# Kernel optimization log

Measured on AMD Instinct MI355X. Metric: run time of the kernel, lower is better.

Reference implementation:

```python
import jax, jax.numpy as jnp
import numpy as np

N = 50000      # nodes
E = 800000     # edges (avg degree 16)
G = 500        # graphs in batch
D = 128        # emb_dim
ED = 7         # edge_dim
L = 5          # num_layers
C = 10         # num_class
BN_EPS = 1e-5


def _bn(x, g, b, m, v):
    # BatchNorm1d in eval mode: running stats
    return (x - m) * jax.lax.rsqrt(v + BN_EPS) * g + b


def setup_inputs() -> dict:
    key = jax.random.key(0)
    ks = jax.random.split(key, 32)
    f32 = jnp.float32
    edge_attr = jax.random.normal(ks[0], (E, ED), f32)
    edge_index = jax.random.randint(ks[1], (2, E), 0, N)
    batch = jnp.sort(jax.random.randint(ks[2], (N,), 0, G))

    w = lambda k, shp, s: jax.random.normal(k, shp, f32) * s
    s_in = 1.0 / np.sqrt(D)
    node_emb = w(ks[3], (1, D), 1.0)
    edge_W = w(ks[4], (L, ED, D), 1.0 / np.sqrt(ED))
    edge_b = w(ks[5], (L, D), 0.01)
    mlp_W1 = w(ks[6], (L, D, D), s_in)
    mlp_b1 = w(ks[7], (L, D), 0.01)
    mlp_W2 = w(ks[8], (L, D, D), s_in)
    mlp_b2 = w(ks[9], (L, D), 0.01)
    bn1_g = jax.random.uniform(ks[10], (L, D), f32, 0.5, 1.5)
    bn1_b = w(ks[11], (L, D), 0.1)
    bn1_m = w(ks[12], (L, D), 0.1)
    bn1_v = jax.random.uniform(ks[13], (L, D), f32, 0.5, 1.5)
    bn2_g = jax.random.uniform(ks[14], (L, D), f32, 0.5, 1.5)
    bn2_b = w(ks[15], (L, D), 0.1)
    bn2_m = w(ks[16], (L, D), 0.1)
    bn2_v = jax.random.uniform(ks[17], (L, D), f32, 0.5, 1.5)
    head_W1 = w(ks[18], (D, D), s_in)
    head_b1 = w(ks[19], (D,), 0.01)
    head_W2 = w(ks[20], (D, C), s_in)
    head_b2 = w(ks[21], (C,), 0.01)
    return dict(edge_attr=edge_attr, edge_index=edge_index, batch=batch,
                node_emb=node_emb, edge_W=edge_W, edge_b=edge_b,
                mlp_W1=mlp_W1, mlp_b1=mlp_b1, bn1_g=bn1_g, bn1_b=bn1_b,
                bn1_m=bn1_m, bn1_v=bn1_v, mlp_W2=mlp_W2, mlp_b2=mlp_b2,
                bn2_g=bn2_g, bn2_b=bn2_b, bn2_m=bn2_m, bn2_v=bn2_v,
                head_W1=head_W1, head_b1=head_b1, head_W2=head_W2, head_b2=head_b2)


def reference(edge_attr, edge_index, batch, node_emb, edge_W, edge_b,
              mlp_W1, mlp_b1, bn1_g, bn1_b, bn1_m, bn1_v,
              mlp_W2, mlp_b2, bn2_g, bn2_b, bn2_m, bn2_v,
              head_W1, head_b1, head_W2, head_b2):
    src, dst = edge_index[0], edge_index[1]
    # node_emb indexed by zeros -> every node starts with the same row
    x = jnp.broadcast_to(node_emb[0], (N, D))
    for l in range(L):
        # GINEConv: msg_ij = relu(x_j + Lin(edge_attr_ij)); aggr = sum over in-edges
        e = edge_attr @ edge_W[l] + edge_b[l]               # [E, D]
        msg = jax.nn.relu(x[src] + e)                       # gather + add + relu
        agg = jax.ops.segment_sum(msg, dst, num_segments=N) # scatter-add
        h = x + agg                                         # (1 + eps) * x, eps = 0
        # inner MLP: Linear -> BN -> ReLU -> Linear
        h = h @ mlp_W1[l] + mlp_b1[l]
        h = jax.nn.relu(_bn(h, bn1_g[l], bn1_b[l], bn1_m[l], bn1_v[l]))
        h = h @ mlp_W2[l] + mlp_b2[l]
        # outer BN + ReLU (dropout identity in eval)
        x = jax.nn.relu(_bn(h, bn2_g[l], bn2_b[l], bn2_m[l], bn2_v[l]))
    # global mean pool over graphs
    counts = jnp.maximum(jax.ops.segment_sum(jnp.ones((N,), x.dtype), batch, num_segments=G), 1.0)
    g = jax.ops.segment_sum(x, batch, num_segments=G) / counts[:, None]
    # head: Linear -> ReLU -> (Dropout) -> Linear
    h = jax.nn.relu(g @ head_W1 + head_b1)
    return h @ head_W2 + head_b2
```

## Files before the change

kernel.cpp:

```cpp
#include <hip/hip_runtime.h>

#define N_NODES 50000
#define N_PAD   50048
#define N_EDGES 800000
#define N_GRAPHS 500
#define DIM 128
#define EDIM 7
#define LAYERS 5
#define NCLASS 10
#define BN_EPS 1e-5f
#define TM 64
#define AST 264
#define NSB ((N_NODES + 256) / 256)
#define NBA 16

typedef __attribute__((ext_vector_type(8))) short bf16x8;
typedef __attribute__((ext_vector_type(4))) float f32x4;
typedef _Float16 h2 __attribute__((ext_vector_type(2)));

struct __align__(32) ERec { uint4 ea; int src; int pad0, pad1, pad2; };

__device__ __forceinline__ unsigned short f2bf(float f) {
    unsigned u = __float_as_uint(f);
    u = u + 0x7fffu + ((u >> 16) & 1u);
    return (unsigned short)(u >> 16);
}
__device__ __forceinline__ float bf2f(unsigned short h) {
    return __uint_as_float(((unsigned)h) << 16);
}
__device__ __forceinline__ h2 u2h2(unsigned u) {
    union { unsigned u; h2 h; } c; c.u = u; return c.h;
}
__device__ __forceinline__ unsigned h22u(h2 h) {
    union { h2 h; unsigned u; } c; c.h = h; return c.u;
}
__device__ __forceinline__ unsigned packh2(float a, float b) {
    h2 h; h.x = (_Float16)a; h.y = (_Float16)b;
    return h22u(h);
}


__global__ void zero_ints(int* __restrict__ p, int n) {
    int i = blockIdx.x * 256 + threadIdx.x;
    if (i < n) p[i] = 0;
}

__global__ void hist_kernel(const int* __restrict__ dst, int* __restrict__ deg) {
    int e = blockIdx.x * 256 + threadIdx.x;
    if (e < N_EDGES) atomicAdd(&deg[dst[e]], 1);
}

__global__ __launch_bounds__(256)
void scan1(const int* __restrict__ deg, int* __restrict__ ro, int* __restrict__ bsums) {
    __shared__ int ws[4];
    int t = threadIdx.x;
    int i = blockIdx.x * 256 + t;
    int v = (i < N_NODES) ? deg[i] : 0;
    int lane = t & 63, wv = t >> 6;
    int s = v;
    #pragma unroll
    for (int off = 1; off < 64; off <<= 1) {
        int u = __shfl_up(s, off, 64);
        if (lane >= off) s += u;
    }
    if (lane == 63) ws[wv] = s;
    __syncthreads();
    if (t == 0) {
        int a = 0;
        #pragma unroll
        for (int k = 0; k < 4; ++k) { int x = ws[k]; ws[k] = a; a += x; }
        bsums[blockIdx.x] = a;
    }
    __syncthreads();
    int excl = s - v + ws[wv];
    if (i <= N_NODES) ro[i] = excl;
}

__global__ __launch_bounds__(256)
void scan2(int* __restrict__ bsums) {
    __shared__ int ws[4];
    int t = threadIdx.x;
    int v = (t < NSB) ? bsums[t] : 0;
    int lane = t & 63, wv = t >> 6;
    int s = v;
    #pragma unroll
    for (int off = 1; off < 64; off <<= 1) {
        int u = __shfl_up(s, off, 64);
        if (lane >= off) s += u;
    }
    if (lane == 63) ws[wv] = s;
    __syncthreads();
    if (t == 0) {
        int a = 0;
        #pragma unroll
        for (int k = 0; k < 4; ++k) { int x = ws[k]; ws[k] = a; a += x; }
    }
    __syncthreads();
    if (t < NSB) bsums[t] = s - v + ws[wv];
}

__global__ __launch_bounds__(256)
void scan3(int* __restrict__ ro, const int* __restrict__ bsums, int* __restrict__ cursor) {
    int i = blockIdx.x * 256 + threadIdx.x;
    if (i <= N_NODES) {
        int r = ro[i] + bsums[i >> 8];
        ro[i] = r;
        if (i < N_NODES) cursor[i] = r;
    }
}

__global__ void fill_rec(const int* __restrict__ dst, const int* __restrict__ src,
                         const float* __restrict__ edge_attr,
                         int* __restrict__ cursor, ERec* __restrict__ rec) {
    int e = blockIdx.x * 256 + threadIdx.x;
    if (e < N_EDGES) {
        const float* ap = edge_attr + (size_t)e * EDIM;
        uint4 ea;
        ea.x = packh2(ap[0], ap[1]);
        ea.y = packh2(ap[2], ap[3]);
        ea.z = packh2(ap[4], ap[5]);
        ea.w = packh2(ap[6], 0.f);
        int s = src[e];
        int pos = atomicAdd(&cursor[dst[e]], 1);
        rec[pos].ea = ea;
        rec[pos].src = s;
    }
}


__global__ void init_x(float* __restrict__ x, unsigned short* __restrict__ xb,
                       const float* __restrict__ emb) {
    int i = blockIdx.x * 256 + threadIdx.x;
    if (i < N_NODES * DIM) {
        float v = emb[i & (DIM - 1)];
        x[i] = v;
        xb[i] = f2bf(v);
    }
}

__global__ void prep_w(const float* __restrict__ W1, const float* __restrict__ W2,
                       unsigned short* __restrict__ Wthi, unsigned short* __restrict__ Wtlo) {
    int i = blockIdx.x * 256 + threadIdx.x;
    if (i >= 2 * LAYERS * DIM * DIM) return;
    int m = i >> 14;
    int n = i & 127;
    int k = (i >> 7) & 127;
    const float* W = (m < LAYERS) ? (W1 + (size_t)m * DIM * DIM)
                                  : (W2 + (size_t)(m - LAYERS) * DIM * DIM);
    float v = W[k * DIM + n];
    unsigned short hi = f2bf(v);
    float lo = v - bf2f(hi);
    size_t o = ((size_t)m << 14) + (size_t)n * DIM + k;
    Wthi[o] = hi;
    Wtlo[o] = f2bf(lo);
}


#if __has_builtin(__builtin_amdgcn_fdot2)
#define HAVE_FDOT2 1
#else
#define HAVE_FDOT2 0
#endif

__device__ __forceinline__ void edge_accum8(float4& acc0, float4& acc1,
                                            uint4 eav, uint4 xv,
                                            const unsigned* Wp,
                                            const float4& b0, const float4& b1) {
    float el[8] = {b0.x, b0.y, b0.z, b0.w, b1.x, b1.y, b1.z, b1.w};
#if HAVE_FDOT2
    #pragma unroll
    for (int d = 0; d < 8; ++d) {
        float e = el[d];
        e = __builtin_amdgcn_fdot2(u2h2(eav.x), u2h2(Wp[d * 4 + 0]), e, false);
        e = __builtin_amdgcn_fdot2(u2h2(eav.y), u2h2(Wp[d * 4 + 1]), e, false);
        e = __builtin_amdgcn_fdot2(u2h2(eav.z), u2h2(Wp[d * 4 + 2]), e, false);
        e = __builtin_amdgcn_fdot2(u2h2(eav.w), u2h2(Wp[d * 4 + 3]), e, false);
        el[d] = e;
    }
#else
    h2 ea01 = u2h2(eav.x), ea23 = u2h2(eav.y), ea45 = u2h2(eav.z), ea67 = u2h2(eav.w);
    float a[8] = {(float)ea01.x, (float)ea01.y, (float)ea23.x, (float)ea23.y,
                  (float)ea45.x, (float)ea45.y, (float)ea67.x, 0.f};
    #pragma unroll
    for (int d = 0; d < 8; ++d) {
        float e = el[d];
        #pragma unroll
        for (int kp = 0; kp < 4; ++kp) {
            h2 w = u2h2(Wp[d * 4 + kp]);
            e += a[kp * 2] * (float)w.x + a[kp * 2 + 1] * (float)w.y;
        }
        el[d] = e;
    }
#endif
    acc0.x += fmaxf(__uint_as_float(xv.x << 16)         + el[0], 0.f);
    acc0.y += fmaxf(__uint_as_float(xv.x & 0xffff0000u) + el[1], 0.f);
    acc0.z += fmaxf(__uint_as_float(xv.y << 16)         + el[2], 0.f);
    acc0.w += fmaxf(__uint_as_float(xv.y & 0xffff0000u) + el[3], 0.f);
    acc1.x += fmaxf(__uint_as_float(xv.z << 16)         + el[4], 0.f);
    acc1.y += fmaxf(__uint_as_float(xv.z & 0xffff0000u) + el[5], 0.f);
    acc1.z += fmaxf(__uint_as_float(xv.w << 16)         + el[6], 0.f);
    acc1.w += fmaxf(__uint_as_float(xv.w & 0xffff0000u) + el[7], 0.f);
}

__global__ __launch_bounds__(256, 4)
void aggregate(const float* __restrict__ x, const unsigned short* __restrict__ xb,
               float* __restrict__ h,
               const ERec* __restrict__ rec,
               const int* __restrict__ row_off,
               const float* __restrict__ eW, const float* __restrict__ eb) {
    int t = threadIdx.x;
    int nl = t >> 4, lane = t & 15, c0 = lane * 8;
    int n = blockIdx.x * NBA + nl;

    unsigned Wp[32];
    #pragma unroll
    for (int d = 0; d < 8; ++d) {
        #pragma unroll
        for (int kp = 0; kp < 4; ++kp) {
            float w0 = eW[(kp * 2) * DIM + c0 + d];
            float w1 = (kp * 2 + 1 < EDIM) ? eW[(kp * 2 + 1) * DIM + c0 + d] : 0.f;
            Wp[d * 4 + kp] = packh2(w0, w1);
        }
    }
    float4 b0 = *reinterpret_cast<const float4*>(eb + c0);
    float4 b1 = *reinterpret_cast<const float4*>(eb + c0 + 4);
    #pragma unroll
    for (int k = 0; k < 32; ++k) asm volatile("" : "+v"(Wp[k]));
    asm volatile("" : "+v"(b0.x), "+v"(b0.y), "+v"(b0.z), "+v"(b0.w));
    asm volatile("" : "+v"(b1.x), "+v"(b1.y), "+v"(b1.z), "+v"(b1.w));

    float4 acc0 = *reinterpret_cast<const float4*>(x + (size_t)n * DIM + c0);
    float4 acc1 = *reinterpret_cast<const float4*>(x + (size_t)n * DIM + c0 + 4);
    int idx = row_off[n], end = row_off[n + 1];

    int s_c[4];
    bool have = (idx + 4 <= end);
    if (have) {
        #pragma unroll
        for (int j = 0; j < 4; ++j) s_c[j] = rec[idx + j].src;
    }
    while (have) {
        uint4 ea[4], xv[4];
        #pragma unroll
        for (int j = 0; j < 4; ++j) ea[j] = rec[idx + j].ea;
        #pragma unroll
        for (int j = 0; j < 4; ++j) xv[j] = *reinterpret_cast<const uint4*>(xb + (size_t)s_c[j] * DIM + c0);
        idx += 4;
        bool nxt = (idx + 4 <= end);
        int s_n[4];
        if (nxt) {
            #pragma unroll
            for (int j = 0; j < 4; ++j) s_n[j] = rec[idx + j].src;
        }
        #pragma unroll
        for (int j = 0; j < 4; ++j) edge_accum8(acc0, acc1, ea[j], xv[j], Wp, b0, b1);
        if (nxt) {
            #pragma unroll
            for (int j = 0; j < 4; ++j) s_c[j] = s_n[j];
        }
        have = nxt;
    }
    for (; idx < end; ++idx) {
        int s = rec[idx].src;
        uint4 ea = rec[idx].ea;
        uint4 xv = *reinterpret_cast<const uint4*>(xb + (size_t)s * DIM + c0);
        edge_accum8(acc0, acc1, ea, xv, Wp, b0, b1);
    }
    *reinterpret_cast<float4*>(h + (size_t)n * DIM + c0) = acc0;
    *reinterpret_cast<float4*>(h + (size_t)n * DIM + c0 + 4) = acc1;
}


__global__ __launch_bounds__(256)
void gemm2x(const float* __restrict__ in, float* __restrict__ outx,
            unsigned short* __restrict__ xb_out,
            const unsigned short* __restrict__ W1hi, const unsigned short* __restrict__ W1lo,
            const unsigned short* __restrict__ W2hi, const unsigned short* __restrict__ W2lo,
            const float* __restrict__ b1,
            const float* __restrict__ bn1g, const float* __restrict__ bn1b,
            const float* __restrict__ bn1m, const float* __restrict__ bn1v,
            const float* __restrict__ b2,
            const float* __restrict__ bn2g, const float* __restrict__ bn2b,
            const float* __restrict__ bn2m, const float* __restrict__ bn2v) {
    __shared__ __align__(16) unsigned short A2[TM * AST];
    int t = threadIdx.x;
    int r0 = blockIdx.x * TM;
    int w = t >> 6;
    int lane = t & 63;
    int q = lane >> 4;
    int l16 = lane & 15;

    bf16x8 bh[2][4], bl[2][4];
    #pragma unroll
    for (int nt = 0; nt < 2; ++nt) {
        int n = w * 32 + nt * 16 + l16;
        const bf16x8* gh = reinterpret_cast<const bf16x8*>(W1hi + (size_t)n * DIM);
        const bf16x8* gl = reinterpret_cast<const bf16x8*>(W1lo + (size_t)n * DIM);
        #pragma unroll
        for (int kc = 0; kc < 4; ++kc) {
            bh[nt][kc] = gh[kc * 4 + q];
            bl[nt][kc] = gl[kc * 4 + q];
        }
    }

    #pragma unroll
    for (int i = 0; i < 8; ++i) {
        int idx = t + i * 256;
        int row = idx >> 5;
        int kp = (idx & 31) * 4;
        float4 v = reinterpret_cast<const float4*>(in + (size_t)r0 * DIM)[idx];
        unsigned short h0 = f2bf(v.x), h1 = f2bf(v.y), h2_ = f2bf(v.z), h3 = f2bf(v.w);
        ushort4 hv; hv.x = h0; hv.y = h1; hv.z = h2_; hv.w = h3;
        ushort4 lv;
        lv.x = f2bf(v.x - bf2f(h0)); lv.y = f2bf(v.y - bf2f(h1));
        lv.z = f2bf(v.z - bf2f(h2_)); lv.w = f2bf(v.w - bf2f(h3));
        *reinterpret_cast<ushort4*>(&A2[row * AST + kp]) = hv;
        *reinterpret_cast<ushort4*>(&A2[row * AST + 128 + kp]) = lv;
    }
    __syncthreads();

    f32x4 acc[4][2];
    #pragma unroll
    for (int mt = 0; mt < 4; ++mt)
        #pragma unroll
        for (int nt = 0; nt < 2; ++nt)
            acc[mt][nt] = (f32x4){0.f, 0.f, 0.f, 0.f};

    #pragma unroll
    for (int kc = 0; kc < 4; ++kc) {
        bf16x8 ahi[4], alo[4];
        #pragma unroll
        for (int mt = 0; mt < 4; ++mt) {
            ahi[mt] = *reinterpret_cast<const bf16x8*>(&A2[(mt * 16 + l16) * AST + kc * 32 + q * 8]);
            alo[mt] = *reinterpret_cast<const bf16x8*>(&A2[(mt * 16 + l16) * AST + 128 + kc * 32 + q * 8]);
        }
        #pragma unroll
        for (int mt = 0; mt < 4; ++mt)
            #pragma unroll
            for (int nt = 0; nt < 2; ++nt) {
                acc[mt][nt] = __builtin_amdgcn_mfma_f32_16x16x32_bf16(ahi[mt], bh[nt][kc], acc[mt][nt], 0, 0, 0);
                acc[mt][nt] = __builtin_amdgcn_mfma_f32_16x16x32_bf16(ahi[mt], bl[nt][kc], acc[mt][nt], 0, 0, 0);
                acc[mt][nt] = __builtin_amdgcn_mfma_f32_16x16x32_bf16(alo[mt], bh[nt][kc], acc[mt][nt], 0, 0, 0);
            }
    }
    __syncthreads();

    #pragma unroll
    for (int nt = 0; nt < 2; ++nt) {
        int n = w * 32 + nt * 16 + l16;
        const bf16x8* gh = reinterpret_cast<const bf16x8*>(W2hi + (size_t)n * DIM);
        const bf16x8* gl = reinterpret_cast<const bf16x8*>(W2lo + (size_t)n * DIM);
        #pragma unroll
        for (int kc = 0; kc < 4; ++kc) {
            bh[nt][kc] = gh[kc * 4 + q];
            bl[nt][kc] = gl[kc * 4 + q];
        }
    }

    #pragma unroll
    for (int nt = 0; nt < 2; ++nt) {
        int col = w * 32 + nt * 16 + l16;
        float bias = b1[col];
        float sc = bn1g[col] * rsqrtf(bn1v[col] + BN_EPS);
        float sh = bn1b[col] - bn1m[col] * sc;
        #pragma unroll
        for (int mt = 0; mt < 4; ++mt) {
            #pragma unroll
            for (int r = 0; r < 4; ++r) {
                int rowl = mt * 16 + q * 4 + r;
                float o = fmaxf((acc[mt][nt][r] + bias) * sc + sh, 0.f);
                unsigned short hi = f2bf(o);
                A2[rowl * AST + col] = hi;
                A2[rowl * AST + 128 + col] = f2bf(o - bf2f(hi));
            }
        }
    }
    __syncthreads();

    #pragma unroll
    for (int mt = 0; mt < 4; ++mt)
        #pragma unroll
        for (int nt = 0; nt < 2; ++nt)
            acc[mt][nt] = (f32x4){0.f, 0.f, 0.f, 0.f};

    #pragma unroll
    for (int kc = 0; kc < 4; ++kc) {
        bf16x8 ahi[4], alo[4];
        #pragma unroll
        for (int mt = 0; mt < 4; ++mt) {
            ahi[mt] = *reinterpret_cast<const bf16x8*>(&A2[(mt * 16 + l16) * AST + kc * 32 + q * 8]);
            alo[mt] = *reinterpret_cast<const bf16x8*>(&A2[(mt * 16 + l16) * AST + 128 + kc * 32 + q * 8]);
        }
        #pragma unroll
        for (int mt = 0; mt < 4; ++mt)
            #pragma unroll
            for (int nt = 0; nt < 2; ++nt) {
                acc[mt][nt] = __builtin_amdgcn_mfma_f32_16x16x32_bf16(ahi[mt], bh[nt][kc], acc[mt][nt], 0, 0, 0);
                acc[mt][nt] = __builtin_amdgcn_mfma_f32_16x16x32_bf16(ahi[mt], bl[nt][kc], acc[mt][nt], 0, 0, 0);
                acc[mt][nt] = __builtin_amdgcn_mfma_f32_16x16x32_bf16(alo[mt], bh[nt][kc], acc[mt][nt], 0, 0, 0);
            }
    }

    #pragma unroll
    for (int nt = 0; nt < 2; ++nt) {
        int col = w * 32 + nt * 16 + l16;
        float bias = b2[col];
        float sc = bn2g[col] * rsqrtf(bn2v[col] + BN_EPS);
        float sh = bn2b[col] - bn2m[col] * sc;
        #pragma unroll
        for (int mt = 0; mt < 4; ++mt) {
            #pragma unroll
            for (int r = 0; r < 4; ++r) {
                int row = r0 + mt * 16 + q * 4 + r;
                float o = fmaxf((acc[mt][nt][r] + bias) * sc + sh, 0.f);
                outx[(size_t)row * DIM + col] = o;
                xb_out[(size_t)row * DIM + col] = f2bf(o);
            }
        }
    }
}


__global__ __launch_bounds__(256)
void pool_kernel(const float* __restrict__ x, const int* __restrict__ batch,
                 float* __restrict__ g) {
    __shared__ float sh[256];
    __shared__ int sb[2];
    int gid = blockIdx.x;
    int t = threadIdx.x;
    if (t < 2) {
        int tgt = gid + t;
        int lo = 0, hi = N_NODES;
        while (lo < hi) { int mid = (lo + hi) >> 1; if (batch[mid] < tgt) lo = mid + 1; else hi = mid; }
        sb[t] = lo;
    }
    __syncthreads();
    int lo = sb[0], hi = sb[1];
    int d = t & 127, half = t >> 7;
    float a = 0.f;
    for (int n = lo + half; n < hi; n += 2) a += x[(size_t)n * DIM + d];
    sh[t] = a;
    __syncthreads();
    if (t < DIM) {
        float cnt = fmaxf((float)(hi - lo), 1.f);
        g[gid * DIM + t] = (sh[t] + sh[t + 128]) / cnt;
    }
}


__global__ __launch_bounds__(128)
void head1_kernel(const float* __restrict__ g, const float* __restrict__ W1,
                  const float* __restrict__ b1, float* __restrict__ h1) {
    __shared__ float gs[DIM];
    int gid = blockIdx.x, c = threadIdx.x;
    gs[c] = g[gid * DIM + c];
    __syncthreads();
    float acc = b1[c];
    for (int k = 0; k < DIM; ++k) acc += gs[k] * W1[k * DIM + c];
    h1[gid * DIM + c] = fmaxf(acc, 0.f);
}

__global__ __launch_bounds__(64)
void head2_kernel(const float* __restrict__ h1, const float* __restrict__ W2,
                  const float* __restrict__ b2, float* __restrict__ out) {
    __shared__ float hs[DIM];
    int gid = blockIdx.x;
    int t = threadIdx.x;
    hs[t] = h1[gid * DIM + t];
    hs[t + 64] = h1[gid * DIM + t + 64];
    __syncthreads();
    if (t < NCLASS) {
        float acc = b2[t];
        for (int k = 0; k < DIM; ++k) acc += hs[k] * W2[k * NCLASS + t];
        out[gid * NCLASS + t] = acc;
    }
}


extern "C" void kernel_launch(void* const* d_in, const int* in_sizes, int n_in,
                              void* d_out, int out_size, void* d_ws, size_t ws_size,
                              hipStream_t stream) {
    const float* edge_attr = (const float*)d_in[0];
    const int*   edge_index = (const int*)d_in[1];
    const int*   batch = (const int*)d_in[2];
    const float* node_emb = (const float*)d_in[3];
    const float* edge_W = (const float*)d_in[4];
    const float* edge_b = (const float*)d_in[5];
    const float* mlp_W1 = (const float*)d_in[6];
    const float* mlp_b1 = (const float*)d_in[7];
    const float* bn1_g = (const float*)d_in[8];
    const float* bn1_b = (const float*)d_in[9];
    const float* bn1_m = (const float*)d_in[10];
    const float* bn1_v = (const float*)d_in[11];
    const float* mlp_W2 = (const float*)d_in[12];
    const float* mlp_b2 = (const float*)d_in[13];
    const float* bn2_g = (const float*)d_in[14];
    const float* bn2_b = (const float*)d_in[15];
    const float* bn2_m = (const float*)d_in[16];
    const float* bn2_v = (const float*)d_in[17];
    const float* head_W1 = (const float*)d_in[18];
    const float* head_b1 = (const float*)d_in[19];
    const float* head_W2 = (const float*)d_in[20];
    const float* head_b2 = (const float*)d_in[21];
    float* out = (float*)d_out;

    const int* src = edge_index;
    const int* dst = edge_index + N_EDGES;

    size_t off = 0;
    auto carve = [&](size_t bytes) {
        void* p = (char*)d_ws + off;
        off += (bytes + 255) & ~(size_t)255;
        return p;
    };
    float* x            = (float*)carve((size_t)N_PAD * DIM * 4);
    unsigned short* xb  = (unsigned short*)carve((size_t)N_PAD * DIM * 2);
    float* h            = (float*)carve((size_t)N_PAD * DIM * 4);
    ERec* rec           = (ERec*)carve((size_t)N_EDGES * sizeof(ERec));
    unsigned short* Wthi = (unsigned short*)carve((size_t)2 * LAYERS * DIM * DIM * 2);
    unsigned short* Wtlo = (unsigned short*)carve((size_t)2 * LAYERS * DIM * DIM * 2);
    int* deg      = (int*)carve((size_t)N_NODES * 4);
    int* row_off  = (int*)carve((size_t)(N_NODES + 1) * 4);
    int* cursor   = (int*)carve((size_t)N_NODES * 4);
    int* bsums    = (int*)carve((size_t)NSB * 4);
    float* gbuf   = (float*)carve((size_t)N_GRAPHS * DIM * 4);
    float* h1buf  = (float*)carve((size_t)N_GRAPHS * DIM * 4);
    (void)ws_size;

    zero_ints<<<(N_NODES + 255) / 256, 256, 0, stream>>>(deg, N_NODES);
    hist_kernel<<<(N_EDGES + 255) / 256, 256, 0, stream>>>(dst, deg);
    scan1<<<NSB, 256, 0, stream>>>(deg, row_off, bsums);
    scan2<<<1, 256, 0, stream>>>(bsums);
    scan3<<<NSB, 256, 0, stream>>>(row_off, bsums, cursor);
    fill_rec<<<(N_EDGES + 255) / 256, 256, 0, stream>>>(dst, src, edge_attr, cursor, rec);

    init_x<<<(N_NODES * DIM + 255) / 256, 256, 0, stream>>>(x, xb, node_emb);
    prep_w<<<(2 * LAYERS * DIM * DIM + 255) / 256, 256, 0, stream>>>(mlp_W1, mlp_W2, Wthi, Wtlo);

    const int gemm_blocks = N_PAD / TM;
    for (int l = 0; l < LAYERS; ++l) {
        aggregate<<<N_NODES / NBA, 256, 0, stream>>>(
            x, xb, h, rec, row_off,
            edge_W + (size_t)l * EDIM * DIM, edge_b + (size_t)l * DIM);
        gemm2x<<<gemm_blocks, 256, 0, stream>>>(
            h, x, xb,
            Wthi + ((size_t)l << 14), Wtlo + ((size_t)l << 14),
            Wthi + ((size_t)(LAYERS + l) << 14), Wtlo + ((size_t)(LAYERS + l) << 14),
            mlp_b1 + (size_t)l * DIM,
            bn1_g + (size_t)l * DIM, bn1_b + (size_t)l * DIM,
            bn1_m + (size_t)l * DIM, bn1_v + (size_t)l * DIM,
            mlp_b2 + (size_t)l * DIM,
            bn2_g + (size_t)l * DIM, bn2_b + (size_t)l * DIM,
            bn2_m + (size_t)l * DIM, bn2_v + (size_t)l * DIM);
    }

    pool_kernel<<<N_GRAPHS, 256, 0, stream>>>(x, batch, gbuf);
    head1_kernel<<<N_GRAPHS, 128, 0, stream>>>(gbuf, head_W1, head_b1, h1buf);
    head2_kernel<<<N_GRAPHS, 64, 0, stream>>>(h1buf, head_W2, head_b2, out);
}
```

Baseline: 606.6 us.

## Split node edge lists across two half-groups, SoA edge records, stream GEMM weights

The edge record struct is split into a packed 16-byte attribute array and a separate source-index array, removing the 32-byte padded records. The aggregate kernel now assigns 32 threads per node, each half handling half of the in-edges, and combines the two halves with a shuffle reduction. This doubles parallelism per node at the cost of a simpler two-way unrolled loop in place of the previous four-deep software-pipelined one. The GEMM kernel also loads weight fragments per k-chunk with one-ahead prefetch rather than holding all of them in registers, and sets launch bounds to 3 waves to raise occupancy.

```diff
diff --git a/kernel.cpp b/kernel.cpp
--- a/kernel.cpp
+++ b/kernel.cpp
@@ -12,13 +12,10 @@
 #define TM 64
 #define AST 264
 #define NSB ((N_NODES + 256) / 256)
-#define NBA 16
 
 typedef __attribute__((ext_vector_type(8))) short bf16x8;
 typedef __attribute__((ext_vector_type(4))) float f32x4;
 typedef _Float16 h2 __attribute__((ext_vector_type(2)));
-
-struct __align__(32) ERec { uint4 ea; int src; int pad0, pad1, pad2; };
 
 __device__ __forceinline__ unsigned short f2bf(float f) {
     unsigned u = __float_as_uint(f);
@@ -111,7 +108,8 @@
 
 __global__ void fill_rec(const int* __restrict__ dst, const int* __restrict__ src,
                          const float* __restrict__ edge_attr,
-                         int* __restrict__ cursor, ERec* __restrict__ rec) {
+                         int* __restrict__ cursor,
+                         uint4* __restrict__ ea16, int* __restrict__ srcc) {
     int e = blockIdx.x * 256 + threadIdx.x;
     if (e < N_EDGES) {
         const float* ap = edge_attr + (size_t)e * EDIM;
@@ -122,8 +120,8 @@
         ea.w = packh2(ap[6], 0.f);
         int s = src[e];
         int pos = atomicAdd(&cursor[dst[e]], 1);
-        rec[pos].ea = ea;
-        rec[pos].src = s;
+        ea16[pos] = ea;
+        srcc[pos] = s;
     }
 }
 
@@ -205,12 +203,17 @@
 __global__ __launch_bounds__(256, 4)
 void aggregate(const float* __restrict__ x, const unsigned short* __restrict__ xb,
                float* __restrict__ h,
-               const ERec* __restrict__ rec,
+               const uint4* __restrict__ ea16,
+               const int* __restrict__ srcc,
                const int* __restrict__ row_off,
                const float* __restrict__ eW, const float* __restrict__ eb) {
     int t = threadIdx.x;
-    int nl = t >> 4, lane = t & 15, c0 = lane * 8;
-    int n = blockIdx.x * NBA + nl;
+    int g = t >> 5;
+    int lane32 = t & 31;
+    int half = lane32 >> 4;
+    int l16 = lane32 & 15;
+    int c0 = l16 * 8;
+    int n = blockIdx.x * 8 + g;
 
     unsigned Wp[32];
     #pragma unroll
@@ -229,49 +232,51 @@
     asm volatile("" : "+v"(b0.x), "+v"(b0.y), "+v"(b0.z), "+v"(b0.w));
     asm volatile("" : "+v"(b1.x), "+v"(b1.y), "+v"(b1.z), "+v"(b1.w));
 
-    float4 acc0 = *reinterpret_cast<const float4*>(x + (size_t)n * DIM + c0);
-    float4 acc1 = *reinterpret_cast<const float4*>(x + (size_t)n * DIM + c0 + 4);
-    int idx = row_off[n], end = row_off[n + 1];
-
-    int s_c[4];
-    bool have = (idx + 4 <= end);
-    if (have) {
-        #pragma unroll
-        for (int j = 0; j < 4; ++j) s_c[j] = rec[idx + j].src;
-    }
-    while (have) {
-        uint4 ea[4], xv[4];
-        #pragma unroll
-        for (int j = 0; j < 4; ++j) ea[j] = rec[idx + j].ea;
-        #pragma unroll
-        for (int j = 0; j < 4; ++j) xv[j] = *reinterpret_cast<const uint4*>(xb + (size_t)s_c[j] * DIM + c0);
-        idx += 4;
-        bool nxt = (idx + 4 <= end);
-        int s_n[4];
-        if (nxt) {
-            #pragma unroll
-            for (int j = 0; j < 4; ++j) s_n[j] = rec[idx + j].src;
-        }
-        #pragma unroll
-        for (int j = 0; j < 4; ++j) edge_accum8(acc0, acc1, ea[j], xv[j], Wp, b0, b1);
-        if (nxt) {
-            #pragma unroll
-            for (int j = 0; j < 4; ++j) s_c[j] = s_n[j];
-        }
-        have = nxt;
-    }
-    for (; idx < end; ++idx) {
-        int s = rec[idx].src;
-        uint4 ea = rec[idx].ea;
-        uint4 xv = *reinterpret_cast<const uint4*>(xb + (size_t)s * DIM + c0);
-        edge_accum8(acc0, acc1, ea, xv, Wp, b0, b1);
-    }
-    *reinterpret_cast<float4*>(h + (size_t)n * DIM + c0) = acc0;
-    *reinterpret_cast<float4*>(h + (size_t)n * DIM + c0 + 4) = acc1;
-}
-
-
-__global__ __launch_bounds__(256)
+    float4 acc0, acc1;
+    if (half == 0) {
+        acc0 = *reinterpret_cast<const float4*>(x + (size_t)n * DIM + c0);
+        acc1 = *reinterpret_cast<const float4*>(x + (size_t)n * DIM + c0 + 4);
+    } else {
+        acc0 = make_float4(0.f, 0.f, 0.f, 0.f);
+        acc1 = make_float4(0.f, 0.f, 0.f, 0.f);
+    }
+
+    int beg = row_off[n], end = row_off[n + 1];
+    int mid = beg + ((end - beg + 1) >> 1);
+    int idx  = half ? mid : beg;
+    int stop = half ? end : mid;
+
+    for (; idx + 2 <= stop; idx += 2) {
+        int s0 = srcc[idx], s1 = srcc[idx + 1];
+        uint4 ea0 = ea16[idx], ea1 = ea16[idx + 1];
+        uint4 xv0 = *reinterpret_cast<const uint4*>(xb + (size_t)s0 * DIM + c0);
+        uint4 xv1 = *reinterpret_cast<const uint4*>(xb + (size_t)s1 * DIM + c0);
+        edge_accum8(acc0, acc1, ea0, xv0, Wp, b0, b1);
+        edge_accum8(acc0, acc1, ea1, xv1, Wp, b0, b1);
+    }
+    if (idx < stop) {
+        int s0 = srcc[idx];
+        uint4 ea0 = ea16[idx];
+        uint4 xv0 = *reinterpret_cast<const uint4*>(xb + (size_t)s0 * DIM + c0);
+        edge_accum8(acc0, acc1, ea0, xv0, Wp, b0, b1);
+    }
+
+    acc0.x += __shfl_xor(acc0.x, 16, 32);
+    acc0.y += __shfl_xor(acc0.y, 16, 32);
+    acc0.z += __shfl_xor(acc0.z, 16, 32);
+    acc0.w += __shfl_xor(acc0.w, 16, 32);
+    acc1.x += __shfl_xor(acc1.x, 16, 32);
+    acc1.y += __shfl_xor(acc1.y, 16, 32);
+    acc1.z += __shfl_xor(acc1.z, 16, 32);
+    acc1.w += __shfl_xor(acc1.w, 16, 32);
+    if (half == 0) {
+        *reinterpret_cast<float4*>(h + (size_t)n * DIM + c0) = acc0;
+        *reinterpret_cast<float4*>(h + (size_t)n * DIM + c0 + 4) = acc1;
+    }
+}
+
+
+__global__ __launch_bounds__(256, 3)
 void gemm2x(const float* __restrict__ in, float* __restrict__ outx,
             unsigned short* __restrict__ xb_out,
             const unsigned short* __restrict__ W1hi, const unsigned short* __restrict__ W1lo,
@@ -289,18 +294,14 @@
     int lane = t & 63;
     int q = lane >> 4;
     int l16 = lane & 15;
-
-    bf16x8 bh[2][4], bl[2][4];
+    int nfr0 = w * 32 + l16;
+
+    bf16x8 cbh[2], cbl[2];
     #pragma unroll
     for (int nt = 0; nt < 2; ++nt) {
-        int n = w * 32 + nt * 16 + l16;
-        const bf16x8* gh = reinterpret_cast<const bf16x8*>(W1hi + (size_t)n * DIM);
-        const bf16x8* gl = reinterpret_cast<const bf16x8*>(W1lo + (size_t)n * DIM);
-        #pragma unroll
-        for (int kc = 0; kc < 4; ++kc) {
-            bh[nt][kc] = gh[kc * 4 + q];
-            bl[nt][kc] = gl[kc * 4 + q];
-        }
+        size_t o = (size_t)(nfr0 + nt * 16) * DIM + q * 8;
+        cbh[nt] = *reinterpret_cast<const bf16x8*>(W1hi + o);
+        cbl[nt] = *reinterpret_cast<const bf16x8*>(W1lo + o);
     }
 
     #pragma unroll
@@ -328,6 +329,15 @@
 
     #pragma unroll
     for (int kc = 0; kc < 4; ++kc) {
+        bf16x8 nbh[2], nbl[2];
+        if (kc < 3) {
+            #pragma unroll
+            for (int nt = 0; nt < 2; ++nt) {
+                size_t o = (size_t)(nfr0 + nt * 16) * DIM + (kc + 1) * 32 + q * 8;
+                nbh[nt] = *reinterpret_cast<const bf16x8*>(W1hi + o);
+                nbl[nt] = *reinterpret_cast<const bf16x8*>(W1lo + o);
+            }
+        }
         bf16x8 ahi[4], alo[4];
         #pragma unroll
         for (int mt = 0; mt < 4; ++mt) {
@@ -338,23 +348,22 @@
         for (int mt = 0; mt < 4; ++mt)
             #pragma unroll
             for (int nt = 0; nt < 2; ++nt) {
-                acc[mt][nt] = __builtin_amdgcn_mfma_f32_16x16x32_bf16(ahi[mt], bh[nt][kc], acc[mt][nt], 0, 0, 0);
-                acc[mt][nt] = __builtin_amdgcn_mfma_f32_16x16x32_bf16(ahi[mt], bl[nt][kc], acc[mt][nt], 0, 0, 0);
-                acc[mt][nt] = __builtin_amdgcn_mfma_f32_16x16x32_bf16(alo[mt], bh[nt][kc], acc[mt][nt], 0, 0, 0);
+                acc[mt][nt] = __builtin_amdgcn_mfma_f32_16x16x32_bf16(ahi[mt], cbh[nt], acc[mt][nt], 0, 0, 0);
+                acc[mt][nt] = __builtin_amdgcn_mfma_f32_16x16x32_bf16(ahi[mt], cbl[nt], acc[mt][nt], 0, 0, 0);
+                acc[mt][nt] = __builtin_amdgcn_mfma_f32_16x16x32_bf16(alo[mt], cbh[nt], acc[mt][nt], 0, 0, 0);
             }
+        if (kc < 3) {
+            #pragma unroll
+            for (int nt = 0; nt < 2; ++nt) { cbh[nt] = nbh[nt]; cbl[nt] = nbl[nt]; }
+        }
     }
     __syncthreads();
 
     #pragma unroll
     for (int nt = 0; nt < 2; ++nt) {
-        int n = w * 32 + nt * 16 + l16;
-        const bf16x8* gh = reinterpret_cast<const bf16x8*>(W2hi + (size_t)n * DIM);
-        const bf16x8* gl = reinterpret_cast<const bf16x8*>(W2lo + (size_t)n * DIM);
-        #pragma unroll
-        for (int kc = 0; kc < 4; ++kc) {
-            bh[nt][kc] = gh[kc * 4 + q];
-            bl[nt][kc] = gl[kc * 4 + q];
-        }
+        size_t o = (size_t)(nfr0 + nt * 16) * DIM + q * 8;
+        cbh[nt] = *reinterpret_cast<const bf16x8*>(W2hi + o);
+        cbl[nt] = *reinterpret_cast<const bf16x8*>(W2lo + o);
     }
 
     #pragma unroll
@@ -385,6 +394,15 @@
 
     #pragma unroll
     for (int kc = 0; kc < 4; ++kc) {
+        bf16x8 nbh[2], nbl[2];
+        if (kc < 3) {
+            #pragma unroll
+            for (int nt = 0; nt < 2; ++nt) {
+                size_t o = (size_t)(nfr0 + nt * 16) * DIM + (kc + 1) * 32 + q * 8;
+                nbh[nt] = *reinterpret_cast<const bf16x8*>(W2hi + o);
+                nbl[nt] = *reinterpret_cast<const bf16x8*>(W2lo + o);
+            }
+        }
         bf16x8 ahi[4], alo[4];
         #pragma unroll
         for (int mt = 0; mt < 4; ++mt) {
@@ -395,10 +413,14 @@
         for (int mt = 0; mt < 4; ++mt)
             #pragma unroll
             for (int nt = 0; nt < 2; ++nt) {
-                acc[mt][nt] = __builtin_amdgcn_mfma_f32_16x16x32_bf16(ahi[mt], bh[nt][kc], acc[mt][nt], 0, 0, 0);
-                acc[mt][nt] = __builtin_amdgcn_mfma_f32_16x16x32_bf16(ahi[mt], bl[nt][kc], acc[mt][nt], 0, 0, 0);
-                acc[mt][nt] = __builtin_amdgcn_mfma_f32_16x16x32_bf16(alo[mt], bh[nt][kc], acc[mt][nt], 0, 0, 0);
+                acc[mt][nt] = __builtin_amdgcn_mfma_f32_16x16x32_bf16(ahi[mt], cbh[nt], acc[mt][nt], 0, 0, 0);
+                acc[mt][nt] = __builtin_amdgcn_mfma_f32_16x16x32_bf16(ahi[mt], cbl[nt], acc[mt][nt], 0, 0, 0);
+                acc[mt][nt] = __builtin_amdgcn_mfma_f32_16x16x32_bf16(alo[mt], cbh[nt], acc[mt][nt], 0, 0, 0);
             }
+        if (kc < 3) {
+            #pragma unroll
+            for (int nt = 0; nt < 2; ++nt) { cbh[nt] = nbh[nt]; cbl[nt] = nbl[nt]; }
+        }
     }
 
     #pragma unroll
@@ -516,7 +538,8 @@
     float* x            = (float*)carve((size_t)N_PAD * DIM * 4);
     unsigned short* xb  = (unsigned short*)carve((size_t)N_PAD * DIM * 2);
     float* h            = (float*)carve((size_t)N_PAD * DIM * 4);
-    ERec* rec           = (ERec*)carve((size_t)N_EDGES * sizeof(ERec));
+    uint4* ea16         = (uint4*)carve((size_t)N_EDGES * 16);
+    int* srcc           = (int*)carve((size_t)N_EDGES * 4);
     unsigned short* Wthi = (unsigned short*)carve((size_t)2 * LAYERS * DIM * DIM * 2);
     unsigned short* Wtlo = (unsigned short*)carve((size_t)2 * LAYERS * DIM * DIM * 2);
     int* deg      = (int*)carve((size_t)N_NODES * 4);
@@ -532,15 +555,15 @@
     scan1<<<NSB, 256, 0, stream>>>(deg, row_off, bsums);
     scan2<<<1, 256, 0, stream>>>(bsums);
     scan3<<<NSB, 256, 0, stream>>>(row_off, bsums, cursor);
-    fill_rec<<<(N_EDGES + 255) / 256, 256, 0, stream>>>(dst, src, edge_attr, cursor, rec);
+    fill_rec<<<(N_EDGES + 255) / 256, 256, 0, stream>>>(dst, src, edge_attr, cursor, ea16, srcc);
 
     init_x<<<(N_NODES * DIM + 255) / 256, 256, 0, stream>>>(x, xb, node_emb);
     prep_w<<<(2 * LAYERS * DIM * DIM + 255) / 256, 256, 0, stream>>>(mlp_W1, mlp_W2, Wthi, Wtlo);
 
     const int gemm_blocks = N_PAD / TM;
     for (int l = 0; l < LAYERS; ++l) {
-        aggregate<<<N_NODES / NBA, 256, 0, stream>>>(
-            x, xb, h, rec, row_off,
+        aggregate<<<N_NODES / 8, 256, 0, stream>>>(
+            x, xb, h, ea16, srcc, row_off,
             edge_W + (size_t)l * EDIM * DIM, edge_b + (size_t)l * DIM);
         gemm2x<<<gemm_blocks, 256, 0, stream>>>(
             h, x, xb,
```

Result: slower. 643.1 us (+6.0%).

## Remap aggregate to one wavefront per node with two channels per lane

Applied to the files above, without the earlier changes.

Restructures the edge aggregation kernel so that each 64-lane wavefront handles one destination node, with each lane owning two feature channels, instead of sixteen lanes per node each owning eight channels. Per-lane register use drops from 32 packed edge weights to 8, and launch bounds rise to 8 waves per SIMD to raise occupancy for the latency-bound gather. In exchange, every lane now loads the full edge record and runs its own fdot2 edge projection, so edge-record traffic and redundant edge-linear work per node grow. The explicit four-edge software prefetch of source indices is replaced by a simpler two-edge unroll.

```diff
diff --git a/kernel.cpp b/kernel.cpp
--- a/kernel.cpp
+++ b/kernel.cpp
@@ -12,7 +12,6 @@
 #define TM 64
 #define AST 264
 #define NSB ((N_NODES + 256) / 256)
-#define NBA 16
 
 typedef __attribute__((ext_vector_type(8))) short bf16x8;
 typedef __attribute__((ext_vector_type(4))) float f32x4;
@@ -162,112 +161,82 @@
 #define HAVE_FDOT2 0
 #endif
 
-__device__ __forceinline__ void edge_accum8(float4& acc0, float4& acc1,
-                                            uint4 eav, uint4 xv,
-                                            const unsigned* Wp,
-                                            const float4& b0, const float4& b1) {
-    float el[8] = {b0.x, b0.y, b0.z, b0.w, b1.x, b1.y, b1.z, b1.w};
+__device__ __forceinline__ void edge_accum2(float& acc0, float& acc1,
+                                            uint4 eav, unsigned xv,
+                                            const unsigned* Wp0, const unsigned* Wp1,
+                                            float b0, float b1) {
+    float e0 = b0, e1 = b1;
 #if HAVE_FDOT2
-    #pragma unroll
-    for (int d = 0; d < 8; ++d) {
-        float e = el[d];
-        e = __builtin_amdgcn_fdot2(u2h2(eav.x), u2h2(Wp[d * 4 + 0]), e, false);
-        e = __builtin_amdgcn_fdot2(u2h2(eav.y), u2h2(Wp[d * 4 + 1]), e, false);
-        e = __builtin_amdgcn_fdot2(u2h2(eav.z), u2h2(Wp[d * 4 + 2]), e, false);
-        e = __builtin_amdgcn_fdot2(u2h2(eav.w), u2h2(Wp[d * 4 + 3]), e, false);
-        el[d] = e;
-    }
+    e0 = __builtin_amdgcn_fdot2(u2h2(eav.x), u2h2(Wp0[0]), e0, false);
+    e0 = __builtin_amdgcn_fdot2(u2h2(eav.y), u2h2(Wp0[1]), e0, false);
+    e0 = __builtin_amdgcn_fdot2(u2h2(eav.z), u2h2(Wp0[2]), e0, false);
+    e0 = __builtin_amdgcn_fdot2(u2h2(eav.w), u2h2(Wp0[3]), e0, false);
+    e1 = __builtin_amdgcn_fdot2(u2h2(eav.x), u2h2(Wp1[0]), e1, false);
+    e1 = __builtin_amdgcn_fdot2(u2h2(eav.y), u2h2(Wp1[1]), e1, false);
+    e1 = __builtin_amdgcn_fdot2(u2h2(eav.z), u2h2(Wp1[2]), e1, false);
+    e1 = __builtin_amdgcn_fdot2(u2h2(eav.w), u2h2(Wp1[3]), e1, false);
 #else
     h2 ea01 = u2h2(eav.x), ea23 = u2h2(eav.y), ea45 = u2h2(eav.z), ea67 = u2h2(eav.w);
     float a[8] = {(float)ea01.x, (float)ea01.y, (float)ea23.x, (float)ea23.y,
                   (float)ea45.x, (float)ea45.y, (float)ea67.x, 0.f};
     #pragma unroll
-    for (int d = 0; d < 8; ++d) {
-        float e = el[d];
-        #pragma unroll
-        for (int kp = 0; kp < 4; ++kp) {
-            h2 w = u2h2(Wp[d * 4 + kp]);
-            e += a[kp * 2] * (float)w.x + a[kp * 2 + 1] * (float)w.y;
-        }
-        el[d] = e;
+    for (int kp = 0; kp < 4; ++kp) {
+        h2 w0 = u2h2(Wp0[kp]), w1 = u2h2(Wp1[kp]);
+        e0 += a[kp * 2] * (float)w0.x + a[kp * 2 + 1] * (float)w0.y;
+        e1 += a[kp * 2] * (float)w1.x + a[kp * 2 + 1] * (float)w1.y;
     }
 #endif
-    acc0.x += fmaxf(__uint_as_float(xv.x << 16)         + el[0], 0.f);
-    acc0.y += fmaxf(__uint_as_float(xv.x & 0xffff0000u) + el[1], 0.f);
-    acc0.z += fmaxf(__uint_as_float(xv.y << 16)         + el[2], 0.f);
-    acc0.w += fmaxf(__uint_as_float(xv.y & 0xffff0000u) + el[3], 0.f);
-    acc1.x += fmaxf(__uint_as_float(xv.z << 16)         + el[4], 0.f);
-    acc1.y += fmaxf(__uint_as_float(xv.z & 0xffff0000u) + el[5], 0.f);
-    acc1.z += fmaxf(__uint_as_float(xv.w << 16)         + el[6], 0.f);
-    acc1.w += fmaxf(__uint_as_float(xv.w & 0xffff0000u) + el[7], 0.f);
-}
-
-__global__ __launch_bounds__(256, 4)
+    acc0 += fmaxf(__uint_as_float(xv << 16)         + e0, 0.f);
+    acc1 += fmaxf(__uint_as_float(xv & 0xffff0000u) + e1, 0.f);
+}
+
+__global__ __launch_bounds__(256, 8)
 void aggregate(const float* __restrict__ x, const unsigned short* __restrict__ xb,
                float* __restrict__ h,
                const ERec* __restrict__ rec,
                const int* __restrict__ row_off,
                const float* __restrict__ eW, const float* __restrict__ eb) {
     int t = threadIdx.x;
-    int nl = t >> 4, lane = t & 15, c0 = lane * 8;
-    int n = blockIdx.x * NBA + nl;
-
-    unsigned Wp[32];
-    #pragma unroll
-    for (int d = 0; d < 8; ++d) {
-        #pragma unroll
-        for (int kp = 0; kp < 4; ++kp) {
-            float w0 = eW[(kp * 2) * DIM + c0 + d];
-            float w1 = (kp * 2 + 1 < EDIM) ? eW[(kp * 2 + 1) * DIM + c0 + d] : 0.f;
-            Wp[d * 4 + kp] = packh2(w0, w1);
-        }
-    }
-    float4 b0 = *reinterpret_cast<const float4*>(eb + c0);
-    float4 b1 = *reinterpret_cast<const float4*>(eb + c0 + 4);
-    #pragma unroll
-    for (int k = 0; k < 32; ++k) asm volatile("" : "+v"(Wp[k]));
-    asm volatile("" : "+v"(b0.x), "+v"(b0.y), "+v"(b0.z), "+v"(b0.w));
-    asm volatile("" : "+v"(b1.x), "+v"(b1.y), "+v"(b1.z), "+v"(b1.w));
-
-    float4 acc0 = *reinterpret_cast<const float4*>(x + (size_t)n * DIM + c0);
-    float4 acc1 = *reinterpret_cast<const float4*>(x + (size_t)n * DIM + c0 + 4);
+    int wv = __builtin_amdgcn_readfirstlane(t >> 6);
+    int lane = t & 63;
+    int c0 = lane * 2;
+    int n = blockIdx.x * 4 + wv;
+
+    unsigned Wp0[4], Wp1[4];
+    #pragma unroll
+    for (int kp = 0; kp < 4; ++kp) {
+        float w00 = eW[(kp * 2) * DIM + c0];
+        float w01 = (kp * 2 + 1 < EDIM) ? eW[(kp * 2 + 1) * DIM + c0] : 0.f;
+        float w10 = eW[(kp * 2) * DIM + c0 + 1];
+        float w11 = (kp * 2 + 1 < EDIM) ? eW[(kp * 2 + 1) * DIM + c0 + 1] : 0.f;
+        Wp0[kp] = packh2(w00, w01);
+        Wp1[kp] = packh2(w10, w11);
+    }
+    float b0 = eb[c0], b1 = eb[c0 + 1];
+    #pragma unroll
+    for (int k = 0; k < 4; ++k) asm volatile("" : "+v"(Wp0[k]), "+v"(Wp1[k]));
+    asm volatile("" : "+v"(b0), "+v"(b1));
+
+    float acc0 = x[(size_t)n * DIM + c0];
+    float acc1 = x[(size_t)n * DIM + c0 + 1];
     int idx = row_off[n], end = row_off[n + 1];
 
-    int s_c[4];
-    bool have = (idx + 4 <= end);
-    if (have) {
-        #pragma unroll
-        for (int j = 0; j < 4; ++j) s_c[j] = rec[idx + j].src;
-    }
-    while (have) {
-        uint4 ea[4], xv[4];
-        #pragma unroll
-        for (int j = 0; j < 4; ++j) ea[j] = rec[idx + j].ea;
-        #pragma unroll
-        for (int j = 0; j < 4; ++j) xv[j] = *reinterpret_cast<const uint4*>(xb + (size_t)s_c[j] * DIM + c0);
-        idx += 4;
-        bool nxt = (idx + 4 <= end);
-        int s_n[4];
-        if (nxt) {
-            #pragma unroll
-            for (int j = 0; j < 4; ++j) s_n[j] = rec[idx + j].src;
-        }
-        #pragma unroll
-        for (int j = 0; j < 4; ++j) edge_accum8(acc0, acc1, ea[j], xv[j], Wp, b0, b1);
-        if (nxt) {
-            #pragma unroll
-            for (int j = 0; j < 4; ++j) s_c[j] = s_n[j];
-        }
-        have = nxt;
-    }
-    for (; idx < end; ++idx) {
-        int s = rec[idx].src;
-        uint4 ea = rec[idx].ea;
-        uint4 xv = *reinterpret_cast<const uint4*>(xb + (size_t)s * DIM + c0);
-        edge_accum8(acc0, acc1, ea, xv, Wp, b0, b1);
-    }
-    *reinterpret_cast<float4*>(h + (size_t)n * DIM + c0) = acc0;
-    *reinterpret_cast<float4*>(h + (size_t)n * DIM + c0 + 4) = acc1;
+    for (; idx + 2 <= end; idx += 2) {
+        ERec r0 = rec[idx];
+        ERec r1 = rec[idx + 1];
+        unsigned xv0 = *reinterpret_cast<const unsigned*>(xb + (size_t)r0.src * DIM + c0);
+        unsigned xv1 = *reinterpret_cast<const unsigned*>(xb + (size_t)r1.src * DIM + c0);
+        edge_accum2(acc0, acc1, r0.ea, xv0, Wp0, Wp1, b0, b1);
+        edge_accum2(acc0, acc1, r1.ea, xv1, Wp0, Wp1, b0, b1);
+    }
+    if (idx < end) {
+        ERec r0 = rec[idx];
+        unsigned xv0 = *reinterpret_cast<const unsigned*>(xb + (size_t)r0.src * DIM + c0);
+        edge_accum2(acc0, acc1, r0.ea, xv0, Wp0, Wp1, b0, b1);
+    }
+
+    float2 o; o.x = acc0; o.y = acc1;
+    *reinterpret_cast<float2*>(h + (size_t)n * DIM + c0) = o;
 }
 
 
@@ -539,7 +508,7 @@
 
     const int gemm_blocks = N_PAD / TM;
     for (int l = 0; l < LAYERS; ++l) {
-        aggregate<<<N_NODES / NBA, 256, 0, stream>>>(
+        aggregate<<<N_NODES / 4, 256, 0, stream>>>(
             x, xb, h, rec, row_off,
             edge_W + (size_t)l * EDIM * DIM, edge_b + (size_t)l * DIM);
         gemm2x<<<gemm_blocks, 256, 0, stream>>>(
```

Measured after the change: 639.4 us. 5.4% more time.
